# Kernel optimization log

Measured on AMD Instinct MI355X. Metric: run time of the kernel, lower is better.

## Reference

```python
import jax, jax.numpy as jnp
import numpy as np

B, N, L = 256, 128, 2048
NF, AC, HID = 75, 3, 256
DIM, NHEAD, FPD, NWORD = 128, 8, 679, 8600


def setup_inputs() -> dict:
    key = jax.random.key(0)
    ks = iter(jax.random.split(key, 48))
    rn = lambda *s: jax.random.normal(next(ks), s, dtype=jnp.float32) * 0.05
    d = {}
    d['V'] = jax.random.normal(next(ks), (B, N, NF), dtype=jnp.float32)
    d['A'] = jax.random.uniform(next(ks), (B, AC, N, N), dtype=jnp.float32)
    d['fp'] = jax.random.uniform(next(ks), (B, FPD), dtype=jnp.float32)
    d['mol_size'] = jax.random.randint(next(ks), (B,), 1, N + 1, dtype=jnp.int32)
    d['protein_seq'] = jax.random.randint(next(ks), (B, L), 0, NWORD)
    d['label'] = jax.random.randint(next(ks), (B,), 0, 2)
    # GConv blocks (multi-channel GCN): 75->256, 256->256, 256->256
    d['gc_W1'], d['gc_b1'] = rn(AC, NF, HID), rn(HID)
    d['gc_W2'], d['gc_b2'] = rn(AC, HID, HID), rn(HID)
    d['gc_W3'], d['gc_b3'] = rn(AC, HID, HID), rn(HID)
    # fp linear chain: 679->128, 128->128
    d['fp_W1'], d['fp_b1'] = rn(FPD, DIM), rn(DIM)
    d['fp_W2'], d['fp_b2'] = rn(DIM, DIM), rn(DIM)
    # global attention pooling (per-head node scores) + readout
    d['att_W'] = rn(HID, NHEAD)
    d['ro_W'], d['ro_b'] = rn(HID * NHEAD, DIM), rn(DIM)
    d['emb'] = rn(NWORD, DIM)
    # cross-attention projections
    d['mfp_W'], d['mfp_b'] = rn(DIM, DIM), rn(DIM)
    d['pfp_W'], d['pfp_b'] = rn(DIM, DIM), rn(DIM)
    d['mv_W'], d['mv_b'] = rn(DIM, DIM), rn(DIM)
    d['pv_W'], d['pv_b'] = rn(DIM, DIM), rn(DIM)
    # stacked MLPs (3 layers each, width 2*dim)
    d['mlp1_W'], d['mlp1_b'] = rn(3, 2 * DIM, 2 * DIM), rn(3, 2 * DIM)
    d['mlp2_W'], d['mlp2_b'] = rn(3, 2 * DIM, 2 * DIM), rn(3, 2 * DIM)
    d['out1_W'], d['out1_b'] = rn(2 * DIM, 2), rn(2)
    d['out2_W'], d['out2_b'] = rn(2 * DIM, 2), rn(2)
    return d


def _gconv(V, A, W, b):
    # A: [b,c,n,m], V: [b,m,f], W: [c,f,o]
    AV = jnp.einsum('bcnm,bmf->bcnf', A, V)
    return jax.nn.relu(jnp.einsum('bcnf,cfo->bno', AV, W) + b)


def _cross_attn(hvec, prot_emb, mW, mb, pW, pb):
    # hvec: [b,d]; prot_emb: [b,l,d]
    h = jax.nn.relu(hvec @ mW + mb)                       # [b,d]
    hs = jax.nn.relu(jnp.einsum('bld,de->ble', prot_emb, pW) + pb)  # [b,l,d]
    w = jnp.tanh(jnp.einsum('bd,bld->bl', h, hs))         # [b,l]
    ys = w[..., None] * hs                                 # [b,l,d]
    return jnp.max(ys, axis=1)                             # [b,d]


def reference(V, A, fp, mol_size, protein_seq, label,
              gc_W1, gc_b1, gc_W2, gc_b2, gc_W3, gc_b3,
              fp_W1, fp_b1, fp_W2, fp_b2, att_W, ro_W, ro_b, emb,
              mfp_W, mfp_b, pfp_W, pfp_b, mv_W, mv_b, pv_W, pv_b,
              mlp1_W, mlp1_b, mlp2_W, mlp2_b, out1_W, out1_b, out2_W, out2_b):
    # fp linear chain (dropout = identity at inference)
    fp = jax.nn.relu(fp @ fp_W1 + fp_b1)
    fp = jax.nn.relu(fp @ fp_W2 + fp_b2)
    # graph conv blocks
    Vh = _gconv(V, A, gc_W1, gc_b1)
    Vh = _gconv(Vh, A, gc_W2, gc_b2)
    Vh = _gconv(Vh, A, gc_W3, gc_b3)
    # masked multi-head global attention pooling over nodes
    scores = jnp.einsum('bnf,fh->bnh', Vh, att_W)          # [b,n,heads]
    mask = jnp.arange(N)[None, :] < mol_size[:, None]       # [b,n]
    scores = jnp.where(mask[..., None], scores, -1e9)
    att = jax.nn.softmax(scores, axis=1)
    pooled = jnp.einsum('bnh,bnf->bhf', att, Vh).reshape(Vh.shape[0], -1)  # [b, heads*nf]
    Vr = jax.nn.relu(pooled @ ro_W + ro_b)                  # [b,dim]
    # protein embedding + ragged cross-attention branches
    prot_emb = emb[protein_seq]                             # [b,l,dim]
    itact1 = _cross_attn(fp, prot_emb, mfp_W, mfp_b, pfp_W, pfp_b)
    itact2 = _cross_attn(Vr, prot_emb, mv_W, mv_b, pv_W, pv_b)
    cat1 = jnp.concatenate([fp, itact1], axis=1)
    cat2 = jnp.concatenate([Vr, itact2], axis=1)
    for i in range(mlp1_W.shape[0]):
        cat1 = jax.nn.relu(cat1 @ mlp1_W[i] + mlp1_b[i])
        cat2 = jax.nn.relu(cat2 @ mlp2_W[i] + mlp2_b[i])
    pred_itact = (cat1 @ out1_W + out1_b) + (cat2 @ out2_W + out2_b)
    pred_labels = jnp.argmax(pred_itact, axis=1)
    pred_scores = jax.nn.softmax(pred_itact, axis=1)[:, 1]
    return (pred_itact, label, pred_labels, pred_scores)
```

## Files before the change

kernel.cpp:

```cpp
#include <hip/hip_runtime.h>
#include <math.h>

static constexpr int BB   = 256;
static constexpr int NN   = 128;
static constexpr int LL   = 2048;
static constexpr int NF   = 75;
static constexpr int AC   = 3;
static constexpr int HID  = 256;
static constexpr int DIM  = 128;
static constexpr int NHEAD= 8;
static constexpr int FPD  = 679;
static constexpr int FPDP = 704;
static constexpr int NWORD= 8600;
static constexpr int NWP  = 8704;
static constexpr int KB   = 768;

typedef __attribute__((ext_vector_type(8))) _Float16 f16x8;
typedef __attribute__((ext_vector_type(2))) _Float16 h2v;
typedef __attribute__((ext_vector_type(4))) float f32x4;
typedef unsigned int u32;
typedef unsigned short u16;

__device__ __forceinline__ u16 f2h(float x) {
    _Float16 h = (_Float16)x;
    return *(u16*)&h;
}
__device__ __forceinline__ u16 f2h_sat(float x) {
    x = fminf(fmaxf(x, -65000.f), 65000.f);
    _Float16 h = (_Float16)x;
    return *(u16*)&h;
}
__device__ __forceinline__ float h2f(u16 x) {
    return (float)(*(_Float16*)&x);
}

static constexpr float SC   = 0.0625f;
static constexpr float USC  = 16.0f;

__global__ __launch_bounds__(256)
void prepA_kernel(const float* __restrict__ A, u16* __restrict__ Ah)
{
    size_t base = (size_t)blockIdx.x * (NN * NN);
    int t = threadIdx.x;
    #pragma unroll
    for (int i = 0; i < 16; ++i) {
        int id = t + i * 256;
        float4 v = *(const float4*)(A + base + (size_t)id * 4);
        u32 p0 = (u32)f2h(v.x) | ((u32)f2h(v.y) << 16);
        u32 p1 = (u32)f2h(v.z) | ((u32)f2h(v.w) << 16);
        *(uint2*)(Ah + base + (size_t)id * 4) = make_uint2(p0, p1);
    }
}

__global__ __launch_bounds__(256)
void prepFp_kernel(const float* __restrict__ fp, u16* __restrict__ fph)
{
    int b = blockIdx.x, t = threadIdx.x;
    for (int i = t; i < FPDP; i += 256) {
        float v = (i < FPD) ? fp[(size_t)b * FPD + i] : 0.f;
        fph[(size_t)b * FPDP + i] = f2h(v);
    }
}

__global__ __launch_bounds__(256)
void prepFpW_kernel(const float* __restrict__ fpW1, const float* __restrict__ fpW2,
                    u16* __restrict__ W1t, u16* __restrict__ W2t)
{
    int o = blockIdx.x, z = blockIdx.y, t = threadIdx.x;
    if (z == 0) {
        for (int k = t; k < FPDP; k += 256) {
            float v = (k < FPD) ? fpW1[(size_t)k * DIM + o] : 0.f;
            W1t[(size_t)o * FPDP + k] = f2h(v);
        }
    } else {
        if (t < 128) W2t[(size_t)o * 128 + t] = f2h(fpW2[(size_t)t * DIM + o]);
    }
}

__global__ __launch_bounds__(128)
void prepCrossW_kernel(const float* __restrict__ pfpW, const float* __restrict__ pvW,
                       const float* __restrict__ mfpW, const float* __restrict__ mvW,
                       u16* __restrict__ pWt12, u16* __restrict__ mWt12)
{
    int o = blockIdx.x, z = blockIdx.y, t = threadIdx.x;
    const float* W = (z == 0) ? pfpW : (z == 1) ? pvW : (z == 2) ? mfpW : mvW;
    u16* Wt = (z < 2) ? (pWt12 + (size_t)z * 128 * 128)
                      : (mWt12 + (size_t)(z - 2) * 128 * 128);
    Wt[(size_t)o * 128 + t] = f2h(W[(size_t)t * 128 + o]);
}

__global__ __launch_bounds__(256)
void prepMlpW_kernel(const float* __restrict__ m1W, const float* __restrict__ m2W,
                     u16* __restrict__ Wmlp)
{
    int o = blockIdx.x, Lr = blockIdx.y, br = blockIdx.z, t = threadIdx.x;
    const float* W = (br ? m2W : m1W) + (size_t)Lr * 256 * 256;
    Wmlp[(((size_t)(br * 3 + Lr)) * 256 + o) * 256 + t] = f2h(W[(size_t)t * 256 + o]);
}

__global__ __launch_bounds__(256)
void fp1_mfma(const u16* __restrict__ fph, const u16* __restrict__ W1t,
              const float* __restrict__ b1, u16* __restrict__ FP1h)
{
    __shared__ u16 As[128 * 40];
    __shared__ u16 Bs[128 * 40];
    int mt = blockIdx.x;
    const u16* Ap = fph + (size_t)(mt * 128) * FPDP;

    int t = threadIdx.x;
    int l = t & 63, wid = t >> 6;
    int rb = (wid >> 1) * 64, cb = (wid & 1) * 64;
    int ln = l & 15, q = l >> 4;

    f32x4 acc[4][4] = {};

    for (int kt = 0; kt < FPDP / 32; ++kt) {
        #pragma unroll
        for (int i = 0; i < 2; ++i) {
            int id = t + i * 256;
            int row = id >> 2, qh = id & 3;
            *(uint4*)&As[row * 40 + qh * 8] =
                *(const uint4*)(Ap + (size_t)row * FPDP + kt * 32 + qh * 8);
            *(uint4*)&Bs[row * 40 + qh * 8] =
                *(const uint4*)(W1t + (size_t)row * FPDP + kt * 32 + qh * 8);
        }
        __syncthreads();
        f16x8 af[4], bfr[4];
        #pragma unroll
        for (int fr = 0; fr < 4; ++fr)
            af[fr] = *(const f16x8*)&As[(rb + fr * 16 + ln) * 40 + q * 8];
        #pragma unroll
        for (int fc = 0; fc < 4; ++fc)
            bfr[fc] = *(const f16x8*)&Bs[(cb + fc * 16 + ln) * 40 + q * 8];
        #pragma unroll
        for (int fr = 0; fr < 4; ++fr)
            #pragma unroll
            for (int fc = 0; fc < 4; ++fc)
                acc[fr][fc] = __builtin_amdgcn_mfma_f32_16x16x32_f16(
                    af[fr], bfr[fc], acc[fr][fc], 0, 0, 0);
        __syncthreads();
    }
    #pragma unroll
    for (int fr = 0; fr < 4; ++fr)
        #pragma unroll
        for (int fc = 0; fc < 4; ++fc) {
            int d = cb + fc * 16 + ln;
            float bv = b1[d];
            #pragma unroll
            for (int r = 0; r < 4; ++r) {
                int m = rb + fr * 16 + q * 4 + r;
                FP1h[(size_t)(mt * 128 + m) * 128 + d] = f2h(fmaxf(acc[fr][fc][r] + bv, 0.f));
            }
        }
}

__global__ __launch_bounds__(256)
void fp2_mfma(const u16* __restrict__ FP1h, const u16* __restrict__ W2t,
              const float* __restrict__ b2, float* __restrict__ FP2,
              u16* __restrict__ FP2h)
{
    __shared__ u16 As[128 * 40];
    __shared__ u16 Bs[128 * 40];
    int mt = blockIdx.x;
    const u16* Ap = FP1h + (size_t)(mt * 128) * 128;

    int t = threadIdx.x;
    int l = t & 63, wid = t >> 6;
    int rb = (wid >> 1) * 64, cb = (wid & 1) * 64;
    int ln = l & 15, q = l >> 4;

    f32x4 acc[4][4] = {};

    for (int kt = 0; kt < 4; ++kt) {
        #pragma unroll
        for (int i = 0; i < 2; ++i) {
            int id = t + i * 256;
            int row = id >> 2, qh = id & 3;
            *(uint4*)&As[row * 40 + qh * 8] =
                *(const uint4*)(Ap + (size_t)row * 128 + kt * 32 + qh * 8);
            *(uint4*)&Bs[row * 40 + qh * 8] =
                *(const uint4*)(W2t + (size_t)row * 128 + kt * 32 + qh * 8);
        }
        __syncthreads();
        f16x8 af[4], bfr[4];
        #pragma unroll
        for (int fr = 0; fr < 4; ++fr)
            af[fr] = *(const f16x8*)&As[(rb + fr * 16 + ln) * 40 + q * 8];
        #pragma unroll
        for (int fc = 0; fc < 4; ++fc)
            bfr[fc] = *(const f16x8*)&Bs[(cb + fc * 16 + ln) * 40 + q * 8];
        #pragma unroll
        for (int fr = 0; fr < 4; ++fr)
            #pragma unroll
            for (int fc = 0; fc < 4; ++fc)
                acc[fr][fc] = __builtin_amdgcn_mfma_f32_16x16x32_f16(
                    af[fr], bfr[fc], acc[fr][fc], 0, 0, 0);
        __syncthreads();
    }
    #pragma unroll
    for (int fr = 0; fr < 4; ++fr)
        #pragma unroll
        for (int fc = 0; fc < 4; ++fc) {
            int d = cb + fc * 16 + ln;
            float bv = b2[d];
            #pragma unroll
            for (int r = 0; r < 4; ++r) {
                int m = rb + fr * 16 + q * 4 + r;
                float val = fmaxf(acc[fr][fc][r] + bv, 0.f);
                FP2 [(size_t)(mt * 128 + m) * 128 + d] = val;
                FP2h[(size_t)(mt * 128 + m) * 128 + d] = f2h(val);
            }
        }
}

__global__ __launch_bounds__(256)
void hs12_mfma(const float* __restrict__ emb, const u16* __restrict__ pWt12,
               const float* __restrict__ ba, const float* __restrict__ bb_,
               u16* __restrict__ HS12)
{
    __shared__ u16 As[128 * 40];
    __shared__ u16 Bs[128 * 40];
    int ft = blockIdx.x, br = blockIdx.y;
    const u16* Bp = pWt12 + (size_t)br * 128 * 128;
    const float* bias = br ? bb_ : ba;
    int r0 = ft * 128;

    int t = threadIdx.x;
    int l = t & 63, wid = t >> 6;
    int rb = (wid >> 1) * 64, cb = (wid & 1) * 64;
    int ln = l & 15, q = l >> 4;
// ... 23 lines not shown
        __syncthreads();
        f16x8 af[4], bfr[4];
        #pragma unroll
        for (int fr = 0; fr < 4; ++fr)
            af[fr] = *(const f16x8*)&As[(rb + fr * 16 + ln) * 40 + q * 8];
        #pragma unroll
        for (int fc = 0; fc < 4; ++fc)
            bfr[fc] = *(const f16x8*)&Bs[(cb + fc * 16 + ln) * 40 + q * 8];
        #pragma unroll
        for (int fr = 0; fr < 4; ++fr)
            #pragma unroll
            for (int fc = 0; fc < 4; ++fc)
                acc[fr][fc] = __builtin_amdgcn_mfma_f32_16x16x32_f16(
                    af[fr], bfr[fc], acc[fr][fc], 0, 0, 0);
        __syncthreads();
    }
    #pragma unroll
    for (int fr = 0; fr < 4; ++fr)
        #pragma unroll
        for (int fc = 0; fc < 4; ++fc) {
            int d = cb + fc * 16 + ln;
            float bv = bias[d];
            #pragma unroll
            for (int r = 0; r < 4; ++r) {
                int m = rb + fr * 16 + q * 4 + r;
                int rr = r0 + m;
                if (rr < NWORD)
                    HS12[(size_t)rr * 256 + br * 128 + d] = f2h(fmaxf(acc[fr][fc][r] + bv, 0.f));
            }
        }
}

__global__ __launch_bounds__(256)
void prepVt_kernel(const float* __restrict__ V, u16* __restrict__ Vt)
{
    int b = blockIdx.x, t = threadIdx.x;
    __shared__ float sV[NN * NF];
    for (int i = t; i < NN * NF; i += 256) sV[i] = V[(size_t)b * (NN * NF) + i];
    __syncthreads();
    for (int i = t; i < 80 * 128; i += 256) {
        int f = i >> 7, n = i & 127;
        float v = (f < NF) ? sV[n * NF + f] : 0.f;
        Vt[(size_t)b * (80 * 128) + i] = f2h(v);
    }
}

__global__ __launch_bounds__(256)
void prepW_kernel(const float* __restrict__ W1, const float* __restrict__ W2,
                  const float* __restrict__ W3, u16* __restrict__ Wt1,
                  u16* __restrict__ Wt2, u16* __restrict__ Wt3)
{
    int o = blockIdx.x, z = blockIdx.y, t = threadIdx.x;
    if (z == 0) {
        int k = t;
        int c = k / 80, f = k - c * 80;
        float v = (c < 3 && f < NF) ? W1[((size_t)c * NF + f) * HID + o] : 0.f;
        Wt1[(size_t)o * 256 + k] = f2h(v);
    } else {
        const float* W = (z == 1) ? W2 : W3;
        u16* Wt = (z == 1) ? Wt2 : Wt3;
        for (int k = t; k < KB; k += 256) {
            int c = k >> 8, f = k & 255;
            Wt[(size_t)o * KB + k] = f2h(W[((size_t)c * HID + f) * HID + o]);
        }
    }
}

__global__ __launch_bounds__(256)
void gA_mfma(const u16* __restrict__ Agr, const u16* __restrict__ Htr,
             u16* __restrict__ AV, int b0, int htStride, int fpMul, int Fvalid)
{
    __shared__ u16 As[128 * 40];
    __shared__ u16 Bs[128 * 40];
    int ft = blockIdx.x, c = blockIdx.y, bl = blockIdx.z;
    int b = b0 + bl;
    const u16* Ap = Agr + ((size_t)b * AC + c) * (NN * NN);
    const u16* Bp = Htr + (size_t)b * htStride + ft * (128 * 128);
    u16* Cp = AV + (size_t)bl * (NN * KB) + c * fpMul + ft * 128;

    int t = threadIdx.x;
    int l = t & 63, wid = t >> 6;
    int rb = (wid >> 1) * 64, cb = (wid & 1) * 64;
    int ln = l & 15, q = l >> 4;

    f32x4 acc[4][4] = {};

    for (int kt = 0; kt < 4; ++kt) {
        #pragma unroll
        for (int i = 0; i < 2; ++i) {
            int id = t + i * 256;
            int row = id >> 2, qh = id & 3;
            *(uint4*)&As[row * 40 + qh * 8] =
                *(const uint4*)(Ap + (size_t)row * NN + kt * 32 + qh * 8);
        }
        #pragma unroll
        for (int i = 0; i < 2; ++i) {
            int id = t + i * 256;
            int row = id >> 2, qh = id & 3;
            uint4 v = make_uint4(0, 0, 0, 0);
            if (row < Fvalid) v = *(const uint4*)(Bp + (size_t)row * 128 + kt * 32 + qh * 8);
            *(uint4*)&Bs[row * 40 + qh * 8] = v;
// ... 73 lines not shown
            for (int fr = 0; fr < 4; ++fr)
                af[fr] = *(const f16x8*)&As[kt][(rb + fr * 16 + ln) * 40 + q * 8];
            #pragma unroll
            for (int fc = 0; fc < 4; ++fc)
                bfr[fc] = *(const f16x8*)&Bs[(cb + fc * 16 + ln) * 40 + q * 8];
            #pragma unroll
            for (int fr = 0; fr < 4; ++fr)
                #pragma unroll
                for (int fc = 0; fc < 4; ++fc)
                    acc[fr][fc] = __builtin_amdgcn_mfma_f32_16x16x32_f16(
                        af[fr], bfr[fc], acc[fr][fc], 0, 0, 0);
        }
        #pragma unroll
        for (int fr = 0; fr < 4; ++fr)
            #pragma unroll
            for (int fc = 0; fc < 4; ++fc) {
                int fcol = ft * 128 + cb + fc * 16 + ln;
                #pragma unroll
                for (int r = 0; r < 4; ++r) {
                    int n = rb + fr * 16 + q * 4 + r;
                    Cp0[(size_t)n * KB + fcol] = f2h_sat(acc[fr][fc][r] * SC);
                }
            }
    }
}

__global__ __launch_bounds__(256)
void gB_mfma(const u16* __restrict__ AV, const u16* __restrict__ Wt,
             const float* __restrict__ bias, u16* __restrict__ Hout,
             int b0, int kTiles, int Ks, int mode)
{
    __shared__ u16 As[128 * 40];
    __shared__ u16 Bs[128 * 40];
    __shared__ u16 sLT[128][136];
    int ot = blockIdx.x, bl = blockIdx.y;
    int b = b0 + bl;
    const u16* Ap = AV + (size_t)bl * (NN * KB);
    const u16* Bp = Wt + (size_t)ot * 128 * Ks;

    int t = threadIdx.x;
    int l = t & 63, wid = t >> 6;
    int rb = (wid >> 1) * 64, cb = (wid & 1) * 64;
    int ln = l & 15, q = l >> 4;

    f32x4 acc[4][4] = {};

    for (int kt = 0; kt < kTiles; ++kt) {
        #pragma unroll
        for (int i = 0; i < 2; ++i) {
            int id = t + i * 256;
            int row = id >> 2, qh = id & 3;
            *(uint4*)&As[row * 40 + qh * 8] =
                *(const uint4*)(Ap + (size_t)row * KB + kt * 32 + qh * 8);
            *(uint4*)&Bs[row * 40 + qh * 8] =
                *(const uint4*)(Bp + (size_t)row * Ks + kt * 32 + qh * 8);
        }
        __syncthreads();
        f16x8 af[4], bfr[4];
        #pragma unroll
        for (int fr = 0; fr < 4; ++fr)
            af[fr] = *(const f16x8*)&As[(rb + fr * 16 + ln) * 40 + q * 8];
        #pragma unroll
        for (int fc = 0; fc < 4; ++fc)
            bfr[fc] = *(const f16x8*)&Bs[(cb + fc * 16 + ln) * 40 + q * 8];
        #pragma unroll
        for (int fr = 0; fr < 4; ++fr)
            #pragma unroll
            for (int fc = 0; fc < 4; ++fc)
                acc[fr][fc] = __builtin_amdgcn_mfma_f32_16x16x32_f16(
                    af[fr], bfr[fc], acc[fr][fc], 0, 0, 0);
        __syncthreads();
    }
    if (mode == 0) {
        #pragma unroll
        for (int fr = 0; fr < 4; ++fr)
            #pragma unroll
            for (int fc = 0; fc < 4; ++fc) {
                int oc = cb + fc * 16 + ln;
                float bv = bias[ot * 128 + oc];
                #pragma unroll
                for (int r = 0; r < 4; ++r) {
                    int n = rb + fr * 16 + q * 4 + r;
                    sLT[oc][n] = f2h_sat(fmaxf(acc[fr][fc][r] * USC + bv, 0.f));
                }
            }
        __syncthreads();
        int row = t >> 1, half = t & 1;
        u16* dst = Hout + ((size_t)b * HID + ot * 128 + row) * NN + half * 64;
        #pragma unroll
        for (int j = 0; j < 8; ++j)
            *(uint4*)(dst + j * 8) = *(const uint4*)&sLT[row][half * 64 + j * 8];
    } else {
        #pragma unroll
        for (int fr = 0; fr < 4; ++fr)
            #pragma unroll
            for (int fc = 0; fc < 4; ++fc) {
                int oc = cb + fc * 16 + ln;
                float bv = bias[ot * 128 + oc];
                #pragma unroll
                for (int r = 0; r < 4; ++r) {
                    int n = rb + fr * 16 + q * 4 + r;
                    float val = fmaxf(acc[fr][fc][r] * USC + bv, 0.f);
                    Hout[((size_t)b * NN + n) * HID + ot * 128 + oc] = f2h_sat(val * SC);
                }
            }
    }
}

__global__ __launch_bounds__(256)
void pool_kernel(const u16* __restrict__ H3h,
                 const float* __restrict__ attW,
                 const int* __restrict__ msz,
                 float* __restrict__ pooled)
{
    int b = blockIdx.x, t = threadIdx.x;
    __shared__ u16  sTh[128][264];
    __shared__ float sW[HID * NHEAD];
    __shared__ float sS[NN * NHEAD];
    __shared__ float sP[16][NHEAD][2];
    for (int i = t; i < HID * NHEAD; i += 256) sW[i] = attW[i];
    const u16* Hb = H3h + (size_t)b * NN * HID;
    for (int i = t; i < 128 * 32; i += 256) {
        int row = i >> 5, fq = (i & 31) * 8;
        *(uint4*)&sTh[row][fq] = *(const uint4*)(Hb + (size_t)row * HID + fq);
// ... 176 lines not shown
            p2 += __shfl_xor(p2, off);
        }
        float w1 = 1.f - 2.f / (__expf(2.f * p1) + 1.f);
        float w2 = 1.f - 2.f / (__expf(2.f * p2) + 1.f);
        _Float16 w1s = (_Float16)w1, w2s = (_Float16)w2;
        h2v w1p = (h2v){w1s, w1s}, w2p = (h2v){w2s, w2s};
        #pragma unroll
        for (int k = 0; k < 4; ++k) {
            h2v pr1 = w1p * vap[k];
            h2v pr2 = w2p * vbp[k];
            m1[k] = (h2v){ m1[k][0] > pr1[0] ? m1[k][0] : pr1[0],
                           m1[k][1] > pr1[1] ? m1[k][1] : pr1[1] };
            m2[k] = (h2v){ m2[k][0] > pr2[0] ? m2[k][0] : pr2[0],
                           m2[k][1] > pr2[1] ? m2[k][1] : pr2[1] };
        }
    }
    __shared__ float red[16][2][DIM];
    #pragma unroll
    for (int k = 0; k < 4; ++k) {
        red[g][0][d0 + 2 * k]     = (float)m1[k][0];
        red[g][0][d0 + 2 * k + 1] = (float)m1[k][1];
        red[g][1][d0 + 2 * k]     = (float)m2[k][0];
        red[g][1][d0 + 2 * k + 1] = (float)m2[k][1];
    }
    __syncthreads();
    int tb = t >> 7, d = t & 127;
    float mx = red[0][tb][d];
    #pragma unroll
    for (int gg = 1; gg < 16; ++gg) mx = fmaxf(mx, red[gg][tb][d]);
    Pc[(((size_t)s * BB + b) * 2 + tb) * DIM + d] = mx;
}

__global__ __launch_bounds__(256)
void prepX_kernel(const float* __restrict__ FP2, const float* __restrict__ VR,
                  const float* __restrict__ Pc, u16* __restrict__ Xh)
{
    int b = blockIdx.x, br = blockIdx.y, t = threadIdx.x;
    float v;
    if (t < 128) {
        v = (br ? VR : FP2)[(size_t)b * 128 + t];
    } else {
        int d = t - 128;
        float m = -INFINITY;
        #pragma unroll
        for (int s = 0; s < 8; ++s)
            m = fmaxf(m, Pc[(((size_t)s * BB + b) * 2 + br) * DIM + d]);
        v = m;
    }
    Xh[((size_t)br * BB + b) * 256 + t] = f2h_sat(v * SC);
}

__global__ __launch_bounds__(256)
void mlpL_mfma(const u16* __restrict__ X, const u16* __restrict__ Wmlp,
               const float* __restrict__ m1b, const float* __restrict__ m2b,
               int Lr, u16* __restrict__ Y)
{
    __shared__ u16 As[128 * 40];
    __shared__ u16 Bs[128 * 40];
    int mt = blockIdx.x, ot = blockIdx.y, br = blockIdx.z;
    const u16* Ap = X + ((size_t)br * BB + mt * 128) * 256;
    const u16* Bp = Wmlp + (((size_t)(br * 3 + Lr)) * 256 + ot * 128) * 256;
    const float* bias = (br ? m2b : m1b) + (size_t)Lr * 256 + ot * 128;

    int t = threadIdx.x;
    int l = t & 63, wid = t >> 6;
    int rb = (wid >> 1) * 64, cb = (wid & 1) * 64;
    int ln = l & 15, q = l >> 4;

    f32x4 acc[4][4] = {};

    for (int kt = 0; kt < 8; ++kt) {
        #pragma unroll
        for (int i = 0; i < 2; ++i) {
            int id = t + i * 256;
            int row = id >> 2, qh = id & 3;
            *(uint4*)&As[row * 40 + qh * 8] =
                *(const uint4*)(Ap + (size_t)row * 256 + kt * 32 + qh * 8);
            *(uint4*)&Bs[row * 40 + qh * 8] =
                *(const uint4*)(Bp + (size_t)row * 256 + kt * 32 + qh * 8);
        }
        __syncthreads();
        f16x8 af[4], bfr[4];
        #pragma unroll
        for (int fr = 0; fr < 4; ++fr)
            af[fr] = *(const f16x8*)&As[(rb + fr * 16 + ln) * 40 + q * 8];
        #pragma unroll
        for (int fc = 0; fc < 4; ++fc)
            bfr[fc] = *(const f16x8*)&Bs[(cb + fc * 16 + ln) * 40 + q * 8];
        #pragma unroll
        for (int fr = 0; fr < 4; ++fr)
            #pragma unroll
            for (int fc = 0; fc < 4; ++fc)
                acc[fr][fc] = __builtin_amdgcn_mfma_f32_16x16x32_f16(
                    af[fr], bfr[fc], acc[fr][fc], 0, 0, 0);
        __syncthreads();
    }
    #pragma unroll
    for (int fr = 0; fr < 4; ++fr)
        #pragma unroll
        for (int fc = 0; fc < 4; ++fc) {
            int oc = cb + fc * 16 + ln;
            float bv = bias[oc] * SC;
            #pragma unroll
            for (int r = 0; r < 4; ++r) {
                int m = rb + fr * 16 + q * 4 + r;
                Y[((size_t)br * BB + (mt * 128 + m)) * 256 + ot * 128 + oc] =
                    f2h_sat(fmaxf(acc[fr][fc][r] + bv, 0.f));
            }
        }
}

__global__ __launch_bounds__(256)
void mlp_out_kernel(const u16* __restrict__ Y,
                    const float* __restrict__ o1W, const float* __restrict__ o1b,
                    const float* __restrict__ o2W, const float* __restrict__ o2b,
                    const int* __restrict__ label,
                    float* __restrict__ dout)
{
    int b = blockIdx.x, t = threadIdx.x;
    __shared__ float pl[2][128];
    const u16* y1 = Y + (size_t)b * 256;
    const u16* y2 = Y + ((size_t)BB + b) * 256;
    int j = t & 1, k2 = t >> 1;
    float p = USC * (h2f(y1[k2])       * o1W[k2 * 2 + j]
                   + h2f(y1[k2 + 128]) * o1W[(k2 + 128) * 2 + j]
                   + h2f(y2[k2])       * o2W[k2 * 2 + j]
                   + h2f(y2[k2 + 128]) * o2W[(k2 + 128) * 2 + j]);
    pl[j][k2] = p;
    __syncthreads();
    for (int s = 64; s > 0; s >>= 1) {
        if (k2 < s) pl[j][k2] += pl[j][k2 + s];
        __syncthreads();
    }
    if (t == 0) {
        float l0 = pl[0][0] + o1b[0] + o2b[0];
        float l1 = pl[1][0] + o1b[1] + o2b[1];
        dout[(size_t)b * 2 + 0] = l0;
        dout[(size_t)b * 2 + 1] = l1;
        dout[2 * BB + b] = (float)label[b];
        dout[3 * BB + b] = (float)((l1 > l0) ? 1 : 0);
        float mx = fmaxf(l0, l1);
        float e0 = expf(l0 - mx), e1 = expf(l1 - mx);
// ... 16 lines not shown
    const float* gcW3 = (const float*)d_in[10]; const float* gcb3 = (const float*)d_in[11];
    const float* fpW1 = (const float*)d_in[12]; const float* fpb1 = (const float*)d_in[13];
    const float* fpW2 = (const float*)d_in[14]; const float* fpb2 = (const float*)d_in[15];
    const float* attW = (const float*)d_in[16];
    const float* roW  = (const float*)d_in[17]; const float* rob  = (const float*)d_in[18];
    const float* emb  = (const float*)d_in[19];
    const float* mfpW = (const float*)d_in[20]; const float* mfpb = (const float*)d_in[21];
    const float* pfpW = (const float*)d_in[22]; const float* pfpb = (const float*)d_in[23];
    const float* mvW  = (const float*)d_in[24]; const float* mvb  = (const float*)d_in[25];
    const float* pvW  = (const float*)d_in[26]; const float* pvb  = (const float*)d_in[27];
    const float* m1W  = (const float*)d_in[28]; const float* m1b  = (const float*)d_in[29];
    const float* m2W  = (const float*)d_in[30]; const float* m2b  = (const float*)d_in[31];
    const float* o1W  = (const float*)d_in[32]; const float* o1b  = (const float*)d_in[33];
    const float* o2W  = (const float*)d_in[34]; const float* o2b  = (const float*)d_in[35];
    float* dout = (float*)d_out;

    char* ws = (char*)d_ws;
    size_t off = 0;
    auto alloc = [&](size_t bytes) -> char* {
        char* p = ws + off;
        off += (bytes + 255) & ~(size_t)255;
        return p;
    };
    u16*   Ah    = (u16*)  alloc((size_t)BB * AC * NN * NN * 2);
    u16*   Vt    = (u16*)  alloc((size_t)BB * 80 * 128 * 2);
    u16*   Wt1   = (u16*)  alloc((size_t)256 * 256 * 2);
    u16*   Wt2   = (u16*)  alloc((size_t)256 * KB * 2);
    u16*   Wt3   = (u16*)  alloc((size_t)256 * KB * 2);
    u16*   Ht    = (u16*)  alloc((size_t)BB * HID * NN * 2);
    u16*   H3h   = (u16*)  alloc((size_t)BB * NN * HID * 2);
    u16*   fph   = (u16*)  alloc((size_t)BB * FPDP * 2);
    u16*   W1t   = (u16*)  alloc((size_t)DIM * FPDP * 2);
    u16*   W2t   = (u16*)  alloc((size_t)DIM * DIM * 2);
    u16*   FP1h  = (u16*)  alloc((size_t)BB * DIM * 2);
    float* FP2   = (float*)alloc((size_t)BB * DIM * 4);
    u16*   FP2h  = (u16*)  alloc((size_t)BB * DIM * 2);
    u16*   pWt12 = (u16*)  alloc((size_t)2 * 128 * 128 * 2);
    u16*   mWt12 = (u16*)  alloc((size_t)2 * 128 * 128 * 2);
    u16*   HS12  = (u16*)  alloc((size_t)NWP * 256 * 2);
    float* PO    = (float*)alloc((size_t)BB * HID * NHEAD * 4);
    float* VR    = (float*)alloc((size_t)BB * DIM * 4);
    u16*   VRh   = (u16*)  alloc((size_t)BB * DIM * 2);
    u16*   h1h   = (u16*)  alloc((size_t)BB * DIM * 2);
    u16*   h2h   = (u16*)  alloc((size_t)BB * DIM * 2);
    float* Pc    = (float*)alloc((size_t)8 * BB * 2 * DIM * 4);
    float* Rp    = (float*)alloc((size_t)8 * BB * DIM * 4);
    u16*   Wmlp  = (u16*)  alloc((size_t)2 * 3 * 256 * 256 * 2);
    u16*   Xa    = (u16*)  alloc((size_t)2 * BB * 256 * 2);
    u16*   Xb    = (u16*)  alloc((size_t)2 * BB * 256 * 2);
    size_t fixedBytes = off;

    int CB = 8;
    size_t perB = (size_t)NN * KB * 2;
    {
        const int tiers[] = {256, 128, 64, 32, 16, 8, 4, 2, 1};
        for (int i = 0; i < 9; ++i)
            if (fixedBytes + (size_t)tiers[i] * perB <= ws_size) { CB = tiers[i]; break; }
    }
    u16* AV = (u16*)(ws + fixedBytes);

    prepA_kernel<<<BB * AC, 256, 0, stream>>>(A, Ah);
    prepVt_kernel<<<BB, 256, 0, stream>>>(V, Vt);
    prepW_kernel<<<dim3(256, 3), 256, 0, stream>>>(gcW1, gcW2, gcW3, Wt1, Wt2, Wt3);
    prepFp_kernel<<<BB, 256, 0, stream>>>(fp, fph);
    prepFpW_kernel<<<dim3(128, 2), 256, 0, stream>>>(fpW1, fpW2, W1t, W2t);
    prepCrossW_kernel<<<dim3(128, 4), 128, 0, stream>>>(pfpW, pvW, mfpW, mvW, pWt12, mWt12);
    prepMlpW_kernel<<<dim3(256, 3, 2), 256, 0, stream>>>(m1W, m2W, Wmlp);
    fp1_mfma<<<2, 256, 0, stream>>>(fph, W1t, fpb1, FP1h);
    fp2_mfma<<<2, 256, 0, stream>>>(FP1h, W2t, fpb2, FP2, FP2h);
    hs12_mfma<<<dim3(NWP / 128, 2), 256, 0, stream>>>(emb, pWt12, pfpb, pvb, HS12);

    for (int b0 = 0; b0 < BB; b0 += CB) {
        gA_mfma<<<dim3(1, AC, CB), 256, 0, stream>>>(Ah, Vt, AV, b0, 80 * 128, 80, 80);
        gB_mfma<<<dim3(2, CB), 256, 0, stream>>>(AV, Wt1, gcb1, Ht, b0, 8, 256, 0);
    }
    for (int b0 = 0; b0 < BB; b0 += CB) {
        gA2_mfma<<<dim3(AC, CB), 256, 0, stream>>>(Ah, Ht, AV, b0);
        gB_mfma<<<dim3(2, CB), 256, 0, stream>>>(AV, Wt2, gcb2, Ht, b0, 24, KB, 0);
    }
    for (int b0 = 0; b0 < BB; b0 += CB) {
        gA2_mfma<<<dim3(AC, CB), 256, 0, stream>>>(Ah, Ht, AV, b0);
        gB_mfma<<<dim3(2, CB), 256, 0, stream>>>(AV, Wt3, gcb3, H3h, b0, 24, KB, 1);
    }

    pool_kernel<<<BB, 256, 0, stream>>>(H3h, attW, msz, PO);
    readout_part<<<dim3(BB, 8), 128, 0, stream>>>(PO, roW, Rp);
    readout_merge<<<BB, 128, 0, stream>>>(Rp, rob, VR, VRh);
    atth_mfma<<<dim3(2, 2), 256, 0, stream>>>(FP2h, VRh, mWt12, mfpb, mvb, h1h, h2h);
    cross_part_kernel<<<dim3(BB, 8), 256, 0, stream>>>(seq, HS12, h1h, h2h, Pc);
    prepX_kernel<<<dim3(BB, 2), 256, 0, stream>>>(FP2, VR, Pc, Xa);
    mlpL_mfma<<<dim3(2, 2, 2), 256, 0, stream>>>(Xa, Wmlp, m1b, m2b, 0, Xb);
    mlpL_mfma<<<dim3(2, 2, 2), 256, 0, stream>>>(Xb, Wmlp, m1b, m2b, 1, Xa);
    mlpL_mfma<<<dim3(2, 2, 2), 256, 0, stream>>>(Xa, Wmlp, m1b, m2b, 2, Xb);
    mlp_out_kernel<<<BB, 256, 0, stream>>>(Xb, o1W, o1b, o2W, o2b, lab, dout);
}
```

Baseline: 494.8 us.

## Fuse prep kernels, fp chain, and MLP layers to cut launch count

Merges the weight and fp preparation kernels into one multi-role launch. It fuses the two fp linear layers into one kernel that keeps the intermediate in LDS, and fuses prepX plus the three MLP layers into one kernel that ping-pongs activations in shared memory. It also drops the LDS transpose in the gB_mfma transposed-output epilogue in favour of direct packed 8-byte stores. This removes roughly ten launches and some global round-trips, but the fused MLP runs on only 4 blocks that each do serial work, and the direct stores are less coalesced than the previous LDS-staged 16-byte rows.

Measured after the change: 521.8 us. 5.5% more time.

```diff
diff --git a/kernel.cpp b/kernel.cpp
--- a/kernel.cpp
+++ b/kernel.cpp
@@ -53,57 +53,84 @@
 }
 
 __global__ __launch_bounds__(256)
-void prepFp_kernel(const float* __restrict__ fp, u16* __restrict__ fph)
+void prepVt_kernel(const float* __restrict__ V, u16* __restrict__ Vt)
 {
     int b = blockIdx.x, t = threadIdx.x;
-    for (int i = t; i < FPDP; i += 256) {
-        float v = (i < FPD) ? fp[(size_t)b * FPD + i] : 0.f;
-        fph[(size_t)b * FPDP + i] = f2h(v);
-    }
-}
-
-__global__ __launch_bounds__(256)
-void prepFpW_kernel(const float* __restrict__ fpW1, const float* __restrict__ fpW2,
-                    u16* __restrict__ W1t, u16* __restrict__ W2t)
+    __shared__ float sV[NN * NF];
+    for (int i = t; i < NN * NF; i += 256) sV[i] = V[(size_t)b * (NN * NF) + i];
+    __syncthreads();
+    for (int i = t; i < 80 * 128; i += 256) {
+        int f = i >> 7, n = i & 127;
+        float v = (f < NF) ? sV[n * NF + f] : 0.f;
+        Vt[(size_t)b * (80 * 128) + i] = f2h(v);
+    }
+}
+
+__global__ __launch_bounds__(256)
+void prepAllW_kernel(const float* __restrict__ gcW1, const float* __restrict__ gcW2,
+                     const float* __restrict__ gcW3,
+                     const float* __restrict__ fpW1, const float* __restrict__ fpW2,
+                     const float* __restrict__ pfpW, const float* __restrict__ pvW,
+                     const float* __restrict__ mfpW, const float* __restrict__ mvW,
+                     const float* __restrict__ m1W,  const float* __restrict__ m2W,
+                     const float* __restrict__ fp,
+                     u16* __restrict__ Wt1, u16* __restrict__ Wt2, u16* __restrict__ Wt3,
+                     u16* __restrict__ W1t, u16* __restrict__ W2t,
+                     u16* __restrict__ pWt12, u16* __restrict__ mWt12,
+                     u16* __restrict__ Wmlp, u16* __restrict__ fph)
 {
     int o = blockIdx.x, z = blockIdx.y, t = threadIdx.x;
     if (z == 0) {
-        for (int k = t; k < FPDP; k += 256) {
-            float v = (k < FPD) ? fpW1[(size_t)k * DIM + o] : 0.f;
-            W1t[(size_t)o * FPDP + k] = f2h(v);
-        }
+        int k = t;
+        int c = k / 80, f = k - c * 80;
+        float v = (c < 3 && f < NF) ? gcW1[((size_t)c * NF + f) * HID + o] : 0.f;
+        Wt1[(size_t)o * 256 + k] = f2h(v);
+    } else if (z == 1 || z == 2) {
+        const float* W = (z == 1) ? gcW2 : gcW3;
+        u16* Wt = (z == 1) ? Wt2 : Wt3;
+        for (int k = t; k < KB; k += 256) {
+            int c = k >> 8, f = k & 255;
+            Wt[(size_t)o * KB + k] = f2h(W[((size_t)c * HID + f) * HID + o]);
+        }
+    } else if (z == 3) {
+        if (o < 128) {
+            for (int k = t; k < FPDP; k += 256) {
+                float v = (k < FPD) ? fpW1[(size_t)k * DIM + o] : 0.f;
+                W1t[(size_t)o * FPDP + k] = f2h(v);
+            }
+            if (t < 128) W2t[(size_t)o * 128 + t] = f2h(fpW2[(size_t)t * DIM + o]);
+        }
+    } else if (z == 4) {
+        if (o < 128 && t < 128) {
+            pWt12[(size_t)0 * 16384 + o * 128 + t] = f2h(pfpW[(size_t)t * 128 + o]);
+            pWt12[(size_t)1 * 16384 + o * 128 + t] = f2h(pvW [(size_t)t * 128 + o]);
+            mWt12[(size_t)0 * 16384 + o * 128 + t] = f2h(mfpW[(size_t)t * 128 + o]);
+            mWt12[(size_t)1 * 16384 + o * 128 + t] = f2h(mvW [(size_t)t * 128 + o]);
+        }
+    } else if (z == 5 || z == 6) {
+        int br = z - 5;
+        const float* W = br ? m2W : m1W;
+        #pragma unroll
+        for (int Lr = 0; Lr < 3; ++Lr)
+            Wmlp[(((size_t)(br * 3 + Lr)) * 256 + o) * 256 + t] =
+                f2h(W[(size_t)Lr * 256 * 256 + (size_t)t * 256 + o]);
     } else {
-        if (t < 128) W2t[(size_t)o * 128 + t] = f2h(fpW2[(size_t)t * DIM + o]);
-    }
-}
-
-__global__ __launch_bounds__(128)
-void prepCrossW_kernel(const float* __restrict__ pfpW, const float* __restrict__ pvW,
-                       const float* __restrict__ mfpW, const float* __restrict__ mvW,
-                       u16* __restrict__ pWt12, u16* __restrict__ mWt12)
-{
-    int o = blockIdx.x, z = blockIdx.y, t = threadIdx.x;
-    const float* W = (z == 0) ? pfpW : (z == 1) ? pvW : (z == 2) ? mfpW : mvW;
-    u16* Wt = (z < 2) ? (pWt12 + (size_t)z * 128 * 128)
-                      : (mWt12 + (size_t)(z - 2) * 128 * 128);
-    Wt[(size_t)o * 128 + t] = f2h(W[(size_t)t * 128 + o]);
-}
-
-__global__ __launch_bounds__(256)
-void prepMlpW_kernel(const float* __restrict__ m1W, const float* __restrict__ m2W,
-                     u16* __restrict__ Wmlp)
-{
-    int o = blockIdx.x, Lr = blockIdx.y, br = blockIdx.z, t = threadIdx.x;
-    const float* W = (br ? m2W : m1W) + (size_t)Lr * 256 * 256;
-    Wmlp[(((size_t)(br * 3 + Lr)) * 256 + o) * 256 + t] = f2h(W[(size_t)t * 256 + o]);
-}
-
-__global__ __launch_bounds__(256)
-void fp1_mfma(const u16* __restrict__ fph, const u16* __restrict__ W1t,
-              const float* __restrict__ b1, u16* __restrict__ FP1h)
+        for (int i = t; i < FPDP; i += 256) {
+            float v = (i < FPD) ? fp[(size_t)o * FPD + i] : 0.f;
+            fph[(size_t)o * FPDP + i] = f2h(v);
+        }
+    }
+}
+
+__global__ __launch_bounds__(256)
+void fp12_mfma(const u16* __restrict__ fph, const u16* __restrict__ W1t,
+               const float* __restrict__ b1, const u16* __restrict__ W2t,
+               const float* __restrict__ b2, float* __restrict__ FP2,
+               u16* __restrict__ FP2h)
 {
     __shared__ u16 As[128 * 40];
     __shared__ u16 Bs[128 * 40];
+    __shared__ u16 Xs[128 * 136];
     int mt = blockIdx.x;
     const u16* Ap = fph + (size_t)(mt * 128) * FPDP;
 
@@ -112,23 +139,62 @@
     int rb = (wid >> 1) * 64, cb = (wid & 1) * 64;
     int ln = l & 15, q = l >> 4;
 
+    {
+        f32x4 acc[4][4] = {};
+        for (int kt = 0; kt < FPDP / 32; ++kt) {
+            #pragma unroll
+            for (int i = 0; i < 2; ++i) {
+                int id = t + i * 256;
+                int row = id >> 2, qh = id & 3;
+                *(uint4*)&As[row * 40 + qh * 8] =
+                    *(const uint4*)(Ap + (size_t)row * FPDP + kt * 32 + qh * 8);
+                *(uint4*)&Bs[row * 40 + qh * 8] =
+                    *(const uint4*)(W1t + (size_t)row * FPDP + kt * 32 + qh * 8);
+            }
+            __syncthreads();
+            f16x8 af[4], bfr[4];
+            #pragma unroll
+            for (int fr = 0; fr < 4; ++fr)
+                af[fr] = *(const f16x8*)&As[(rb + fr * 16 + ln) * 40 + q * 8];
+            #pragma unroll
+            for (int fc = 0; fc < 4; ++fc)
+                bfr[fc] = *(const f16x8*)&Bs[(cb + fc * 16 + ln) * 40 + q * 8];
+            #pragma unroll
+            for (int fr = 0; fr < 4; ++fr)
+                #pragma unroll
+                for (int fc = 0; fc < 4; ++fc)
+                    acc[fr][fc] = __builtin_amdgcn_mfma_f32_16x16x32_f16(
+                        af[fr], bfr[fc], acc[fr][fc], 0, 0, 0);
+            __syncthreads();
+        }
+        #pragma unroll
+        for (int fr = 0; fr < 4; ++fr)
+            #pragma unroll
+            for (int fc = 0; fc < 4; ++fc) {
+                int d = cb + fc * 16 + ln;
+                float bv = b1[d];
+                #pragma unroll
+                for (int r = 0; r < 4; ++r) {
+                    int m = rb + fr * 16 + q * 4 + r;
+                    Xs[m * 136 + d] = f2h(fmaxf(acc[fr][fc][r] + bv, 0.f));
+                }
+            }
+    }
     f32x4 acc[4][4] = {};
-
-    for (int kt = 0; kt < FPDP / 32; ++kt) {
+    for (int kt = 0; kt < 4; ++kt) {
+        __syncthreads();
         #pragma unroll
         for (int i = 0; i < 2; ++i) {
             int id = t + i * 256;
             int row = id >> 2, qh = id & 3;
-            *(uint4*)&As[row * 40 + qh * 8] =
-                *(const uint4*)(Ap + (size_t)row * FPDP + kt * 32 + qh * 8);
             *(uint4*)&Bs[row * 40 + qh * 8] =
-                *(const uint4*)(W1t + (size_t)row * FPDP + kt * 32 + qh * 8);
+                *(const uint4*)(W2t + (size_t)row * 128 + kt * 32 + qh * 8);
         }
         __syncthreads();
         f16x8 af[4], bfr[4];
         #pragma unroll
         for (int fr = 0; fr < 4; ++fr)
-            af[fr] = *(const f16x8*)&As[(rb + fr * 16 + ln) * 40 + q * 8];
+            af[fr] = *(const f16x8*)&Xs[(rb + fr * 16 + ln) * 136 + kt * 32 + q * 8];
         #pragma unroll
         for (int fc = 0; fc < 4; ++fc)
             bfr[fc] = *(const f16x8*)&Bs[(cb + fc * 16 + ln) * 40 + q * 8];
@@ -138,64 +204,6 @@
             for (int fc = 0; fc < 4; ++fc)
                 acc[fr][fc] = __builtin_amdgcn_mfma_f32_16x16x32_f16(
                     af[fr], bfr[fc], acc[fr][fc], 0, 0, 0);
-        __syncthreads();
-    }
-    #pragma unroll
-    for (int fr = 0; fr < 4; ++fr)
-        #pragma unroll
-        for (int fc = 0; fc < 4; ++fc) {
-            int d = cb + fc * 16 + ln;
-            float bv = b1[d];
-            #pragma unroll
-            for (int r = 0; r < 4; ++r) {
-                int m = rb + fr * 16 + q * 4 + r;
-                FP1h[(size_t)(mt * 128 + m) * 128 + d] = f2h(fmaxf(acc[fr][fc][r] + bv, 0.f));
-            }
-        }
-}
-
-__global__ __launch_bounds__(256)
-void fp2_mfma(const u16* __restrict__ FP1h, const u16* __restrict__ W2t,
-              const float* __restrict__ b2, float* __restrict__ FP2,
-              u16* __restrict__ FP2h)
-{
-    __shared__ u16 As[128 * 40];
-    __shared__ u16 Bs[128 * 40];
-    int mt = blockIdx.x;
-    const u16* Ap = FP1h + (size_t)(mt * 128) * 128;
-
-    int t = threadIdx.x;
-    int l = t & 63, wid = t >> 6;
-    int rb = (wid >> 1) * 64, cb = (wid & 1) * 64;
-    int ln = l & 15, q = l >> 4;
-
-    f32x4 acc[4][4] = {};
-
-    for (int kt = 0; kt < 4; ++kt) {
-        #pragma unroll
-        for (int i = 0; i < 2; ++i) {
-            int id = t + i * 256;
-            int row = id >> 2, qh = id & 3;
-            *(uint4*)&As[row * 40 + qh * 8] =
-                *(const uint4*)(Ap + (size_t)row * 128 + kt * 32 + qh * 8);
-            *(uint4*)&Bs[row * 40 + qh * 8] =
-                *(const uint4*)(W2t + (size_t)row * 128 + kt * 32 + qh * 8);
-        }
-        __syncthreads();
-        f16x8 af[4], bfr[4];
-        #pragma unroll
-        for (int fr = 0; fr < 4; ++fr)
-            af[fr] = *(const f16x8*)&As[(rb + fr * 16 + ln) * 40 + q * 8];
-        #pragma unroll
-        for (int fc = 0; fc < 4; ++fc)
-            bfr[fc] = *(const f16x8*)&Bs[(cb + fc * 16 + ln) * 40 + q * 8];
-        #pragma unroll
-        for (int fr = 0; fr < 4; ++fr)
-            #pragma unroll
-            for (int fc = 0; fc < 4; ++fc)
-                acc[fr][fc] = __builtin_amdgcn_mfma_f32_16x16x32_f16(
-                    af[fr], bfr[fc], acc[fr][fc], 0, 0, 0);
-        __syncthreads();
     }
     #pragma unroll
     for (int fr = 0; fr < 4; ++fr)
@@ -285,41 +293,6 @@
 }
 
 __global__ __launch_bounds__(256)
-void prepVt_kernel(const float* __restrict__ V, u16* __restrict__ Vt)
-{
-    int b = blockIdx.x, t = threadIdx.x;
-    __shared__ float sV[NN * NF];
-    for (int i = t; i < NN * NF; i += 256) sV[i] = V[(size_t)b * (NN * NF) + i];
-    __syncthreads();
-    for (int i = t; i < 80 * 128; i += 256) {
-        int f = i >> 7, n = i & 127;
-        float v = (f < NF) ? sV[n * NF + f] : 0.f;
-        Vt[(size_t)b * (80 * 128) + i] = f2h(v);
-    }
-}
-
-__global__ __launch_bounds__(256)
-void prepW_kernel(const float* __restrict__ W1, const float* __restrict__ W2,
-                  const float* __restrict__ W3, u16* __restrict__ Wt1,
-                  u16* __restrict__ Wt2, u16* __restrict__ Wt3)
-{
-    int o = blockIdx.x, z = blockIdx.y, t = threadIdx.x;
-    if (z == 0) {
-        int k = t;
-        int c = k / 80, f = k - c * 80;
-        float v = (c < 3 && f < NF) ? W1[((size_t)c * NF + f) * HID + o] : 0.f;
-        Wt1[(size_t)o * 256 + k] = f2h(v);
-    } else {
-        const float* W = (z == 1) ? W2 : W3;
-        u16* Wt = (z == 1) ? Wt2 : Wt3;
-        for (int k = t; k < KB; k += 256) {
-            int c = k >> 8, f = k & 255;
-            Wt[(size_t)o * KB + k] = f2h(W[((size_t)c * HID + f) * HID + o]);
-        }
-    }
-}
-
-__global__ __launch_bounds__(256)
 void gA_mfma(const u16* __restrict__ Agr, const u16* __restrict__ Htr,
              u16* __restrict__ AV, int b0, int htStride, int fpMul, int Fvalid)
 {
@@ -459,7 +432,6 @@
 {
     __shared__ u16 As[128 * 40];
     __shared__ u16 Bs[128 * 40];
-    __shared__ u16 sLT[128][136];
     int ot = blockIdx.x, bl = blockIdx.y;
     int b = b0 + bl;
     const u16* Ap = AV + (size_t)bl * (NN * KB);
@@ -505,18 +477,15 @@
             for (int fc = 0; fc < 4; ++fc) {
                 int oc = cb + fc * 16 + ln;
                 float bv = bias[ot * 128 + oc];
-                #pragma unroll
-                for (int r = 0; r < 4; ++r) {
-                    int n = rb + fr * 16 + q * 4 + r;
-                    sLT[oc][n] = f2h_sat(fmaxf(acc[fr][fc][r] * USC + bv, 0.f));
-                }
-            }
-        __syncthreads();
-        int row = t >> 1, half = t & 1;
-        u16* dst = Hout + ((size_t)b * HID + ot * 128 + row) * NN + half * 64;
-        #pragma unroll
-        for (int j = 0; j < 8; ++j)
-            *(uint4*)(dst + j * 8) = *(const uint4*)&sLT[row][half * 64 + j * 8];
+                int n0 = rb + fr * 16 + q * 4;
+                u16 v0 = f2h_sat(fmaxf(acc[fr][fc][0] * USC + bv, 0.f));
+                u16 v1 = f2h_sat(fmaxf(acc[fr][fc][1] * USC + bv, 0.f));
+                u16 v2 = f2h_sat(fmaxf(acc[fr][fc][2] * USC + bv, 0.f));
+                u16 v3 = f2h_sat(fmaxf(acc[fr][fc][3] * USC + bv, 0.f));
+                uint2 pk = make_uint2((u32)v0 | ((u32)v1 << 16),
+                                      (u32)v2 | ((u32)v3 << 16));
+                *(uint2*)(Hout + ((size_t)b * HID + ot * 128 + oc) * NN + n0) = pk;
+            }
     } else {
         #pragma unroll
         for (int fr = 0; fr < 4; ++fr)
@@ -759,82 +728,89 @@
 }
 
 __global__ __launch_bounds__(256)
-void prepX_kernel(const float* __restrict__ FP2, const float* __restrict__ VR,
-                  const float* __restrict__ Pc, u16* __restrict__ Xh)
-{
-    int b = blockIdx.x, br = blockIdx.y, t = threadIdx.x;
-    float v;
-    if (t < 128) {
-        v = (br ? VR : FP2)[(size_t)b * 128 + t];
-    } else {
-        int d = t - 128;
-        float m = -INFINITY;
-        #pragma unroll
-        for (int s = 0; s < 8; ++s)
-            m = fmaxf(m, Pc[(((size_t)s * BB + b) * 2 + br) * DIM + d]);
-        v = m;
-    }
-    Xh[((size_t)br * BB + b) * 256 + t] = f2h_sat(v * SC);
-}
-
-__global__ __launch_bounds__(256)
-void mlpL_mfma(const u16* __restrict__ X, const u16* __restrict__ Wmlp,
+void mlp3_mfma(const float* __restrict__ FP2, const float* __restrict__ VR,
+               const float* __restrict__ Pc, const u16* __restrict__ Wmlp,
                const float* __restrict__ m1b, const float* __restrict__ m2b,
-               int Lr, u16* __restrict__ Y)
-{
-    __shared__ u16 As[128 * 40];
+               u16* __restrict__ Yf)
+{
+    __shared__ u16 XY[2][128 * 264];
     __shared__ u16 Bs[128 * 40];
-    int mt = blockIdx.x, ot = blockIdx.y, br = blockIdx.z;
-    const u16* Ap = X + ((size_t)br * BB + mt * 128) * 256;
-    const u16* Bp = Wmlp + (((size_t)(br * 3 + Lr)) * 256 + ot * 128) * 256;
-    const float* bias = (br ? m2b : m1b) + (size_t)Lr * 256 + ot * 128;
-
+    int mt = blockIdx.x, br = blockIdx.y;
     int t = threadIdx.x;
+
+    for (int i = t; i < 128 * 256; i += 256) {
+        int row = i >> 8, col = i & 255;
+        int b = mt * 128 + row;
+        float v;
+        if (col < 128) {
+            v = (br ? VR : FP2)[(size_t)b * 128 + col];
+        } else {
+            int d = col - 128;
+            float m = -INFINITY;
+            #pragma unroll
+            for (int s = 0; s < 8; ++s)
+                m = fmaxf(m, Pc[(((size_t)s * BB + b) * 2 + br) * DIM + d]);
+            v = m;
+        }
+        XY[0][row * 264 + col] = f2h_sat(v * SC);
+    }
+
     int l = t & 63, wid = t >> 6;
     int rb = (wid >> 1) * 64, cb = (wid & 1) * 64;
     int ln = l & 15, q = l >> 4;
 
-    f32x4 acc[4][4] = {};
-
-    for (int kt = 0; kt < 8; ++kt) {
-        #pragma unroll
-        for (int i = 0; i < 2; ++i) {
-            int id = t + i * 256;
-            int row = id >> 2, qh = id & 3;
-            *(uint4*)&As[row * 40 + qh * 8] =
-                *(const uint4*)(Ap + (size_t)row * 256 + kt * 32 + qh * 8);
-            *(uint4*)&Bs[row * 40 + qh * 8] =
-                *(const uint4*)(Bp + (size_t)row * 256 + kt * 32 + qh * 8);
-        }
-        __syncthreads();
-        f16x8 af[4], bfr[4];
-        #pragma unroll
-        for (int fr = 0; fr < 4; ++fr)
-            af[fr] = *(const f16x8*)&As[(rb + fr * 16 + ln) * 40 + q * 8];
-        #pragma unroll
-        for (int fc = 0; fc < 4; ++fc)
-            bfr[fc] = *(const f16x8*)&Bs[(cb + fc * 16 + ln) * 40 + q * 8];
-        #pragma unroll
-        for (int fr = 0; fr < 4; ++fr)
-            #pragma unroll
-            for (int fc = 0; fc < 4; ++fc)
-                acc[fr][fc] = __builtin_amdgcn_mfma_f32_16x16x32_f16(
-                    af[fr], bfr[fc], acc[fr][fc], 0, 0, 0);
-        __syncthreads();
-    }
-    #pragma unroll
-    for (int fr = 0; fr < 4; ++fr)
-        #pragma unroll
-        for (int fc = 0; fc < 4; ++fc) {
-            int oc = cb + fc * 16 + ln;
-            float bv = bias[oc] * SC;
-            #pragma unroll
-            for (int r = 0; r < 4; ++r) {
-                int m = rb + fr * 16 + q * 4 + r;
-                Y[((size_t)br * BB + (mt * 128 + m)) * 256 + ot * 128 + oc] =
-                    f2h_sat(fmaxf(acc[fr][fc][r] + bv, 0.f));
-            }
-        }
+    int cur = 0;
+    for (int Lr = 0; Lr < 3; ++Lr) {
+        const float* bias = (br ? m2b : m1b) + (size_t)Lr * 256;
+        for (int ot = 0; ot < 2; ++ot) {
+            const u16* Bp = Wmlp + (((size_t)(br * 3 + Lr)) * 256 + ot * 128) * 256;
+            f32x4 acc[4][4] = {};
+            for (int kt = 0; kt < 8; ++kt) {
+                __syncthreads();
+                #pragma unroll
+                for (int i = 0; i < 2; ++i) {
+                    int id = t + i * 256;
+                    int row = id >> 2, qh = id & 3;
+                    *(uint4*)&Bs[row * 40 + qh * 8] =
+                        *(const uint4*)(Bp + (size_t)row * 256 + kt * 32 + qh * 8);
+                }
+                __syncthreads();
+                f16x8 af[4], bfr[4];
+                #pragma unroll
+                for (int fr = 0; fr < 4; ++fr)
+                    af[fr] = *(const f16x8*)&XY[cur][(rb + fr * 16 + ln) * 264 + kt * 32 + q * 8];
+                #pragma unroll
+                for (int fc = 0; fc < 4; ++fc)
+                    bfr[fc] = *(const f16x8*)&Bs[(cb + fc * 16 + ln) * 40 + q * 8];
+                #pragma unroll
+                for (int fr = 0; fr < 4; ++fr)
+                    #pragma unroll
+                    for (int fc = 0; fc < 4; ++fc)
+                        acc[fr][fc] = __builtin_amdgcn_mfma_f32_16x16x32_f16(
+                            af[fr], bfr[fc], acc[fr][fc], 0, 0, 0);
+            }
+            #pragma unroll
+            for (int fr = 0; fr < 4; ++fr)
+                #pragma unroll
+                for (int fc = 0; fc < 4; ++fc) {
+                    int oc = cb + fc * 16 + ln;
+                    float bv = bias[ot * 128 + oc] * SC;
+                    #pragma unroll
+                    for (int r = 0; r < 4; ++r) {
+                        int m = rb + fr * 16 + q * 4 + r;
+                        XY[cur ^ 1][m * 264 + ot * 128 + oc] =
+                            f2h_sat(fmaxf(acc[fr][fc][r] + bv, 0.f));
+                    }
+                }
+        }
+        cur ^= 1;
+    }
+    __syncthreads();
+    for (int i = t; i < 128 * 32; i += 256) {
+        int row = i >> 5, c8 = (i & 31) * 8;
+        *(uint4*)(Yf + ((size_t)br * BB + mt * 128 + row) * 256 + c8) =
+            *(const uint4*)&XY[cur][row * 264 + c8];
+    }
 }
 
 __global__ __launch_bounds__(256)
@@ -917,7 +893,6 @@
     u16*   fph   = (u16*)  alloc((size_t)BB * FPDP * 2);
     u16*   W1t   = (u16*)  alloc((size_t)DIM * FPDP * 2);
     u16*   W2t   = (u16*)  alloc((size_t)DIM * DIM * 2);
-    u16*   FP1h  = (u16*)  alloc((size_t)BB * DIM * 2);
     float* FP2   = (float*)alloc((size_t)BB * DIM * 4);
     u16*   FP2h  = (u16*)  alloc((size_t)BB * DIM * 2);
     u16*   pWt12 = (u16*)  alloc((size_t)2 * 128 * 128 * 2);
@@ -931,8 +906,7 @@
     float* Pc    = (float*)alloc((size_t)8 * BB * 2 * DIM * 4);
     float* Rp    = (float*)alloc((size_t)8 * BB * DIM * 4);
     u16*   Wmlp  = (u16*)  alloc((size_t)2 * 3 * 256 * 256 * 2);
-    u16*   Xa    = (u16*)  alloc((size_t)2 * BB * 256 * 2);
-    u16*   Xb    = (u16*)  alloc((size_t)2 * BB * 256 * 2);
+    u16*   Yf    = (u16*)  alloc((size_t)2 * BB * 256 * 2);
     size_t fixedBytes = off;
 
     int CB = 8;
@@ -946,13 +920,10 @@
 
     prepA_kernel<<<BB * AC, 256, 0, stream>>>(A, Ah);
     prepVt_kernel<<<BB, 256, 0, stream>>>(V, Vt);
-    prepW_kernel<<<dim3(256, 3), 256, 0, stream>>>(gcW1, gcW2, gcW3, Wt1, Wt2, Wt3);
-    prepFp_kernel<<<BB, 256, 0, stream>>>(fp, fph);
-    prepFpW_kernel<<<dim3(128, 2), 256, 0, stream>>>(fpW1, fpW2, W1t, W2t);
-    prepCrossW_kernel<<<dim3(128, 4), 128, 0, stream>>>(pfpW, pvW, mfpW, mvW, pWt12, mWt12);
-    prepMlpW_kernel<<<dim3(256, 3, 2), 256, 0, stream>>>(m1W, m2W, Wmlp);
-    fp1_mfma<<<2, 256, 0, stream>>>(fph, W1t, fpb1, FP1h);
-    fp2_mfma<<<2, 256, 0, stream>>>(FP1h, W2t, fpb2, FP2, FP2h);
+    prepAllW_kernel<<<dim3(256, 8), 256, 0, stream>>>(
+        gcW1, gcW2, gcW3, fpW1, fpW2, pfpW, pvW, mfpW, mvW, m1W, m2W, fp,
+        Wt1, Wt2, Wt3, W1t, W2t, pWt12, mWt12, Wmlp, fph);
+    fp12_mfma<<<2, 256, 0, stream>>>(fph, W1t, fpb1, W2t, fpb2, FP2, FP2h);
     hs12_mfma<<<dim3(NWP / 128, 2), 256, 0, stream>>>(emb, pWt12, pfpb, pvb, HS12);
 
     for (int b0 = 0; b0 < BB; b0 += CB) {
@@ -973,9 +944,6 @@
     readout_merge<<<BB, 128, 0, stream>>>(Rp, rob, VR, VRh);
     atth_mfma<<<dim3(2, 2), 256, 0, stream>>>(FP2h, VRh, mWt12, mfpb, mvb, h1h, h2h);
     cross_part_kernel<<<dim3(BB, 8), 256, 0, stream>>>(seq, HS12, h1h, h2h, Pc);
-    prepX_kernel<<<dim3(BB, 2), 256, 0, stream>>>(FP2, VR, Pc, Xa);
-    mlpL_mfma<<<dim3(2, 2, 2), 256, 0, stream>>>(Xa, Wmlp, m1b, m2b, 0, Xb);
-    mlpL_mfma<<<dim3(2, 2, 2), 256, 0, stream>>>(Xb, Wmlp, m1b, m2b, 1, Xa);
-    mlpL_mfma<<<dim3(2, 2, 2), 256, 0, stream>>>(Xa, Wmlp, m1b, m2b, 2, Xb);
-    mlp_out_kernel<<<BB, 256, 0, stream>>>(Xb, o1W, o1b, o2W, o2b, lab, dout);
-}
+    mlp3_mfma<<<dim3(2, 2), 256, 0, stream>>>(FP2, VR, Pc, Wmlp, m1b, m2b, Yf);
+    mlp_out_kernel<<<BB, 256, 0, stream>>>(Yf, o1W, o1b, o2W, o2b, lab, dout);
+}
```
